# Kernel tuning notes

Hardware: AMD Instinct MI355X
Metric: run time of the kernel (lower is better)

The kernel has to match this reference:

```python
import jax, jax.numpy as jnp
import numpy as np

D_MODEL = 1024
NUM_HEADS = 16
DEPTH = D_MODEL // NUM_HEADS
B, S = 4, 1024


def setup_inputs() -> dict:
    key = jax.random.key(0)
    ks = jax.random.split(key, 9)
    scale = 0.02
    return {
        "v": jax.random.normal(ks[0], (B, S, D_MODEL), jnp.float32),
        "k": jax.random.normal(ks[1], (B, S, D_MODEL), jnp.float32),
        "q": jax.random.normal(ks[2], (B, S, D_MODEL), jnp.float32),
        "wq_w": jax.random.normal(ks[3], (D_MODEL, D_MODEL), jnp.float32) * scale,
        "wq_b": jax.random.normal(ks[4], (D_MODEL,), jnp.float32) * scale,
        "wv_w": jax.random.normal(ks[5], (D_MODEL, D_MODEL), jnp.float32) * scale,
        "wv_b": jax.random.normal(ks[6], (D_MODEL,), jnp.float32) * scale,
        "dense_w": jax.random.normal(ks[7], (D_MODEL, D_MODEL), jnp.float32) * scale,
        "dense_b": jax.random.normal(ks[8], (D_MODEL,), jnp.float32) * scale,
    }


def _split_heads(x):
    # [B, S, D] -> [B, H, S, depth]
    b, s, _ = x.shape
    return x.reshape(b, s, NUM_HEADS, DEPTH).transpose(0, 2, 1, 3)


def reference(v, k, q, wq_w, wq_b, wv_w, wv_b, dense_w, dense_b):
    # Faithful to original torch module, including its bugs:
    #   v = wv(v); k = wv(v)  (k input and wk layer unused)
    #   output = logits @ v   (raw logits, NOT softmax weights)
    del k  # unused in original forward (overwritten)
    q_p = q @ wq_w.T + wq_b
    v_p = v @ wv_w.T + wv_b
    k_p = v_p @ wv_w.T + wv_b  # k = self.wv(v) after v already projected

    qh = _split_heads(q_p)  # [B,H,S,dh]
    kh = _split_heads(k_p)
    vh = _split_heads(v_p)

    logits = jnp.einsum("bhsd,bhtd->bhst", qh, kh) / jnp.sqrt(
        jnp.asarray(DEPTH, jnp.float32)
    )  # [B,H,S,S]
    attention_weights = jax.nn.softmax(logits, axis=-1)
    # BUG preserved: uses logits, not attention_weights
    attn_out = jnp.einsum("bhst,bhtd->bhsd", logits, vh)  # [B,H,S,dh]

    concat = attn_out.transpose(0, 2, 1, 3).reshape(B, S, D_MODEL)
    output = concat @ dense_w.T + dense_b
    # dropout is identity in eval mode
    return output, attention_weights
```

## Files before the change

### kernel.cpp

```cpp
#include <hip/hip_runtime.h>
#include <hip/hip_bf16.h>

#define DM 1024
#define BS 4
#define SS 1024
#define NH 16

typedef __attribute__((ext_vector_type(8))) short bf16x8;
typedef __attribute__((ext_vector_type(4))) float f32x4;

__device__ inline unsigned short f2bf(float x) {
    union { float f; unsigned u; } v; v.f = x;
    unsigned r = v.u + 0x7fffu + ((v.u >> 16) & 1u);
    return (unsigned short)(r >> 16);
}
__device__ inline float bf2f(unsigned short u) {
    union { unsigned u; float f; } v; v.u = ((unsigned)u) << 16;
    return v.f;
}

template<typename T> __device__ inline void store1(T* p, float v);
template<> __device__ inline void store1<float>(float* p, float v) { *p = v; }
template<> __device__ inline void store1<unsigned short>(unsigned short* p, float v) { *p = f2bf(v); }

__device__ inline void glds16(const unsigned short* g, unsigned short* l) {
    __builtin_amdgcn_global_load_lds(
        (const __attribute__((address_space(1))) unsigned int*)g,
        (__attribute__((address_space(3))) unsigned int*)l, 16, 0, 0);
}

__device__ inline void cvt4(const float* src, unsigned short* dst, long long off) {
    float4 v = reinterpret_cast<const float4*>(src)[off];
    ushort4 o;
    o.x = f2bf(v.x); o.y = f2bf(v.y); o.z = f2bf(v.z); o.w = f2bf(v.w);
    reinterpret_cast<ushort4*>(dst)[off] = o;
}

__global__ __launch_bounds__(256) void cvt4_bf16(
    const float* __restrict__ q, const float* __restrict__ v,
    const float* __restrict__ wq, const float* __restrict__ wv,
    unsigned short* __restrict__ qb, unsigned short* __restrict__ vb,
    unsigned short* __restrict__ wqb, unsigned short* __restrict__ wvb)
{
    const long long NQ = (long long)BS * SS * DM / 4;
    const long long NW = (long long)DM * DM / 4;
    const long long total = 2 * NQ + 2 * NW;
    long long i = (long long)blockIdx.x * 256 + threadIdx.x;
    const long long stride = (long long)gridDim.x * 256;
    for (; i < total; i += stride) {
        if (i < NQ)                cvt4(q, qb, i);
        else if (i < 2 * NQ)       cvt4(v, vb, i - NQ);
        else if (i < 2 * NQ + NW)  cvt4(wq, wqb, i - 2 * NQ);
        else                       cvt4(wv, wvb, i - 2 * NQ - NW);
    }
}

__global__ __launch_bounds__(256) void cvt_bf16(const float* __restrict__ in,
                                                unsigned short* __restrict__ out, int n4)
{
    int i = blockIdx.x * blockDim.x + threadIdx.x;
    const int stride = gridDim.x * blockDim.x;
    for (; i < n4; i += stride) cvt4(in, out, i);
}

template<typename TO>
__global__ __launch_bounds__(256) void gemmb_bt(
    const unsigned short* __restrict__ A, int lda, long long sAb, long long sAh,
    const unsigned short* __restrict__ B, int ldb, long long sBb, long long sBh,
    TO* __restrict__ C, int ldc, long long sCb, long long sCh,
    const float* __restrict__ bias, int K, int H, float scale)
{
    __shared__ unsigned short lA[2][128 * 64];
    __shared__ unsigned short lB[2][64 * 64];

    const int tid = threadIdx.x;
    const int wid = tid >> 6, lane = tid & 63;
    const int wr = wid >> 1, wc = wid & 1;
    const int r0 = lane & 15;
    const int kq = (lane >> 4) * 8;
    const int srow = lane >> 3;
    const int scol = (lane & 7) * 8;

    const int z = blockIdx.z, zb = z / H, zh = z % H;
    const unsigned short* Ap = A + sAb * zb + sAh * zh
        + ((long long)blockIdx.y * 128 + srow) * lda + scol;
    const unsigned short* Bp = B + sBb * zb + sBh * zh
        + ((long long)blockIdx.x * 64 + srow) * ldb + scol;
    TO* Cp = C + sCb * zb + sCh * zh
        + (long long)blockIdx.y * 128 * ldc + blockIdx.x * 64;

    f32x4 acc[4][2];
    #pragma unroll
    for (int m = 0; m < 4; ++m)
        #pragma unroll
        for (int n = 0; n < 2; ++n)
            acc[m][n] = f32x4{0.f, 0.f, 0.f, 0.f};

    #pragma unroll
    for (int k = 0; k < 4; ++k)
        glds16(Ap + (long long)(wid * 32 + k * 8) * lda, &lA[0][(wid * 32 + k * 8) * 64]);
    #pragma unroll
    for (int k = 0; k < 2; ++k)
        glds16(Bp + (long long)(wid * 16 + k * 8) * ldb, &lB[0][(wid * 16 + k * 8) * 64]);
    __syncthreads();

    const int NT = K / 64;
    int cur = 0;
    for (int t = 0; t < NT; ++t) {
        if (t + 1 < NT) {
            #pragma unroll
            for (int k = 0; k < 4; ++k)
                glds16(Ap + (long long)(wid * 32 + k * 8) * lda + (t + 1) * 64,
                       &lA[cur ^ 1][(wid * 32 + k * 8) * 64]);
            #pragma unroll
            for (int k = 0; k < 2; ++k)
                glds16(Bp + (long long)(wid * 16 + k * 8) * ldb + (t + 1) * 64,
                       &lB[cur ^ 1][(wid * 16 + k * 8) * 64]);
        }
        #pragma unroll
        for (int ks = 0; ks < 2; ++ks) {
            bf16x8 af[4], bfr[2];
            #pragma unroll
            for (int m = 0; m < 4; ++m)
                af[m] = *reinterpret_cast<const bf16x8*>(
                    &lA[cur][(wr * 64 + m * 16 + r0) * 64 + ks * 32 + kq]);
            #pragma unroll
            for (int n = 0; n < 2; ++n)
                bfr[n] = *reinterpret_cast<const bf16x8*>(
                    &lB[cur][(wc * 32 + n * 16 + r0) * 64 + ks * 32 + kq]);
            #pragma unroll
            for (int m = 0; m < 4; ++m)
                #pragma unroll
                for (int n = 0; n < 2; ++n)
                    acc[m][n] = __builtin_amdgcn_mfma_f32_16x16x32_bf16(af[m], bfr[n], acc[m][n], 0, 0, 0);
        }
        __syncthreads();
        cur ^= 1;
    }

    const int cf = lane & 15, rf = (lane >> 4) * 4;
    #pragma unroll
    for (int m = 0; m < 4; ++m) {
        #pragma unroll
        for (int n = 0; n < 2; ++n) {
            int col = wc * 32 + n * 16 + cf;
            float bv = bias ? bias[blockIdx.x * 64 + col] : 0.0f;
            #pragma unroll
            for (int j = 0; j < 4; ++j) {
                int row = wr * 64 + m * 16 + rf + j;
                store1<TO>(&Cp[(long long)row * ldc + col], acc[m][n][j] * scale + bv);
            }
        }
    }
}

__global__ __launch_bounds__(256) void transpose_vh(const unsigned short* __restrict__ vp,
                                                    unsigned short* __restrict__ vT)
{
    __shared__ unsigned short tile[64][65];
    const int bh = blockIdx.y;
    const int b = bh >> 4, h = bh & 15;
    const long long t0 = (long long)blockIdx.x * 64;
    const int tid = threadIdx.x;
    #pragma unroll
    for (int kk = 0; kk < 4; ++kk) {
        int l = tid + kk * 256;
        int row = l >> 4, c4 = l & 15;
        const unsigned short* src = vp + ((long long)b * SS + t0 + row) * DM + h * 64 + c4 * 4;
        ushort4 val = *reinterpret_cast<const ushort4*>(src);
        tile[row][c4 * 4 + 0] = val.x;
        tile[row][c4 * 4 + 1] = val.y;
        tile[row][c4 * 4 + 2] = val.z;
        tile[row][c4 * 4 + 3] = val.w;
    }
    __syncthreads();
    #pragma unroll
    for (int kk = 0; kk < 4; ++kk) {
        int l = tid + kk * 256;
        int d = l >> 4, i4 = l & 15;
        ushort4 o;
        o.x = tile[i4 * 4 + 0][d];
        o.y = tile[i4 * 4 + 1][d];
        o.z = tile[i4 * 4 + 2][d];
        o.w = tile[i4 * 4 + 3][d];
        *reinterpret_cast<ushort4*>(vT + ((long long)bh * 64 + d) * SS + t0 + i4 * 4) = o;
    }
}

__global__ __launch_bounds__(512, 4) void fused_attn7(
    const unsigned short* __restrict__ qp,
    const unsigned short* __restrict__ kp,
    const unsigned short* __restrict__ vT,
    float* __restrict__ attnw,
    unsigned short* __restrict__ cc)
{
    constexpr int LSTR = 1032;
    __shared__ alignas(16) unsigned short S16[32 * LSTR];
    __shared__ float sW[8][32];
    __shared__ float rowI[32];

    const int tid = threadIdx.x;
    const int w = tid >> 6;
    const int lane = tid & 63;
    const int lg = lane >> 4;
    const int ln = lane & 15;
    const int z = blockIdx.y, b = z >> 4, h = z & 15;
    const int row0 = blockIdx.x * 32;

    const unsigned short* qbase = qp + ((long long)b * SS + row0) * DM + h * 64;
    const unsigned short* kbase = kp + (long long)b * SS * DM + h * 64;
    const unsigned short* vbase = vT + (long long)z * 64 * SS;

    bf16x8 qf[2][2];
    #pragma unroll
    for (int rh = 0; rh < 2; ++rh)
        #pragma unroll
        for (int ks = 0; ks < 2; ++ks)
            qf[rh][ks] = *reinterpret_cast<const bf16x8*>(
                qbase + (long long)(rh * 16 + ln) * DM + ks * 32 + lg * 8);

    float s4[2][4];
    #pragma unroll
    for (int rh = 0; rh < 2; ++rh)
        #pragma unroll
        for (int j = 0; j < 4; ++j) s4[rh][j] = 0.f;

    bf16x8 kf_cur[4];
    #pragma unroll
    for (int i = 0; i < 4; ++i) {
        const int ks = i >> 1, cf2 = i & 1;
        kf_cur[i] = *reinterpret_cast<const bf16x8*>(
            kbase + (long long)(w * 32 + cf2 * 16 + ln) * DM + ks * 32 + lg * 8);
    }
    for (int c = 0; c < 4; ++c) {
        bf16x8 kf_nxt[4];
        if (c < 3) {
            #pragma unroll
            for (int i = 0; i < 4; ++i) {
                const int ks = i >> 1, cf2 = i & 1;
                kf_nxt[i] = *reinterpret_cast<const bf16x8*>(
                    kbase + (long long)((c + 1) * 256 + w * 32 + cf2 * 16 + ln) * DM + ks * 32 + lg * 8);
            }
        }
        f32x4 sac[2][2];
        #pragma unroll
        for (int rh = 0; rh < 2; ++rh) {
            sac[rh][0] = f32x4{0.f, 0.f, 0.f, 0.f};
            sac[rh][1] = f32x4{0.f, 0.f, 0.f, 0.f};
        }
        #pragma unroll
        for (int ks = 0; ks < 2; ++ks)
            #pragma unroll
            for (int cf2 = 0; cf2 < 2; ++cf2)
                #pragma unroll
                for (int rh = 0; rh < 2; ++rh)
                    sac[rh][cf2] = __builtin_amdgcn_mfma_f32_16x16x32_bf16(
                        qf[rh][ks], kf_cur[ks * 2 + cf2], sac[rh][cf2], 0, 0, 0);

        const int colbase = c * 256 + w * 32;
        #pragma unroll
        for (int rh = 0; rh < 2; ++rh) {
            #pragma unroll
            for (int cf2 = 0; cf2 < 2; ++cf2)
                #pragma unroll
                for (int j = 0; j < 4; ++j) {
                    unsigned short ub = f2bf(sac[rh][cf2][j] * 0.125f);
                    S16[(rh * 16 + lg * 4 + j) * LSTR + colbase + cf2 * 16 + ln] = ub;
                    sac[rh][cf2][j] = bf2f(ub);
                }
            #pragma unroll
            for (int j = 0; j < 4; ++j)
                s4[rh][j] += __expf(sac[rh][0][j]) + __expf(sac[rh][1][j]);
        }
        if (c < 3) {
            #pragma unroll
            for (int i = 0; i < 4; ++i) kf_cur[i] = kf_nxt[i];
        }
    }

    #pragma unroll
    for (int rh = 0; rh < 2; ++rh)
        #pragma unroll
        for (int j = 0; j < 4; ++j) {
            #pragma unroll
            for (int o = 1; o < 16; o <<= 1)
                s4[rh][j] += __shfl_xor(s4[rh][j], o);
        }
    if (ln == 0) {
        #pragma unroll
        for (int rh = 0; rh < 2; ++rh)
            #pragma unroll
            for (int j = 0; j < 4; ++j)
                sW[w][rh * 16 + lg * 4 + j] = s4[rh][j];
    }
    __syncthreads();
    if (tid < 32) {
        float sf = 0.f;
        #pragma unroll
        for (int w2 = 0; w2 < 8; ++w2) sf += sW[w2][tid];
        rowI[tid] = 1.0f / sf;
    }
    __syncthreads();

    {
        const int rh = w >> 2, ds = w & 3;
        f32x4 pvn = f32x4{0.f, 0.f, 0.f, 0.f};
        const unsigned short* vrow = vbase + (long long)(ds * 16 + ln) * SS;
        for (int kk = 0; kk < 32; ++kk) {
            bf16x8 sa = *reinterpret_cast<const bf16x8*>(&S16[(rh * 16 + ln) * LSTR + kk * 32 + lg * 8]);
            bf16x8 vf = *reinterpret_cast<const bf16x8*>(vrow + kk * 32 + lg * 8);
            pvn = __builtin_amdgcn_mfma_f32_16x16x32_bf16(sa, vf, pvn, 0, 0, 0);
        }
        #pragma unroll
        for (int j = 0; j < 4; ++j)
            cc[((long long)b * SS + row0 + rh * 16 + lg * 4 + j) * DM + h * 64 + ds * 16 + ln] = f2bf(pvn[j]);
    }

    {
        const int rr = tid >> 8;
        const int tcol = tid & 255;
        #pragma unroll 4
        for (int it = 0; it < 16; ++it) {
            const int row = it * 2 + rr;
            float inv = rowI[row];
            uint2 sv = *reinterpret_cast<const uint2*>(&S16[row * LSTR + tcol * 4]);
            f32x4 o;
            o[0] = __expf(bf2f((unsigned short)(sv.x & 0xffffu))) * inv;
            o[1] = __expf(bf2f((unsigned short)(sv.x >> 16))) * inv;
            o[2] = __expf(bf2f((unsigned short)(sv.y & 0xffffu))) * inv;
            o[3] = __expf(bf2f((unsigned short)(sv.y >> 16))) * inv;
            __builtin_nontemporal_store(
                o, reinterpret_cast<f32x4*>(attnw + ((long long)z * SS + row0 + row) * SS + tcol * 4));
        }
    }
}

extern "C" void kernel_launch(void* const* d_in, const int* in_sizes, int n_in,
                              void* d_out, int out_size, void* d_ws, size_t ws_size,
                              hipStream_t stream) {
    (void)in_sizes; (void)n_in; (void)out_size;
    const float* v    = (const float*)d_in[0];
    const float* q    = (const float*)d_in[2];
    const float* wq_w = (const float*)d_in[3];
    const float* wq_b = (const float*)d_in[4];
    const float* wv_w = (const float*)d_in[5];
    const float* wv_b = (const float*)d_in[6];
    const float* dw   = (const float*)d_in[7];
    const float* db   = (const float*)d_in[8];

    unsigned short* q_p = (unsigned short*)d_ws;
    unsigned short* v_p = q_p + (4 << 20);
    unsigned short* k_p = v_p + (4 << 20);
    unsigned short* vT  = k_p + (4 << 20);
    unsigned short* cc  = vT  + (4 << 20);

    float* out0   = (float*)d_out;
    float* attnw  = out0 + (long long)BS * SS * DM;

    unsigned short* qb  = (unsigned short*)attnw;
    unsigned short* vb  = qb  + (4 << 20);
    unsigned short* wqb = vb  + (4 << 20);
    unsigned short* wvb = wqb + (1 << 20);

    const bool big_ws = ws_size >= (size_t)(42u << 20);
    unsigned short* dwb = big_ws ? (cc + (4 << 20)) : q_p;

    dim3 blk(256);
    dim3 projGrid(DM / 64, BS * SS / 128, 1);

    cvt4_bf16<<<dim3(2048), blk, 0, stream>>>(q, v, wq_w, wv_w, qb, vb, wqb, wvb);
    if (big_ws)
        cvt_bf16<<<dim3(256), blk, 0, stream>>>(dw, dwb, (DM * DM) / 4);

    gemmb_bt<unsigned short><<<projGrid, blk, 0, stream>>>(
        qb, DM, 0, 0, wqb, DM, 0, 0, q_p, DM, 0, 0, wq_b, DM, 1, 1.0f);
    gemmb_bt<unsigned short><<<projGrid, blk, 0, stream>>>(
        vb, DM, 0, 0, wvb, DM, 0, 0, v_p, DM, 0, 0, wv_b, DM, 1, 1.0f);
    gemmb_bt<unsigned short><<<projGrid, blk, 0, stream>>>(
        v_p, DM, 0, 0, wvb, DM, 0, 0, k_p, DM, 0, 0, wv_b, DM, 1, 1.0f);

    transpose_vh<<<dim3(16, 64), blk, 0, stream>>>(v_p, vT);

    fused_attn7<<<dim3(SS / 32, BS * NH), dim3(512), 0, stream>>>(q_p, k_p, vT, attnw, cc);

    if (!big_ws)
        cvt_bf16<<<dim3(256), blk, 0, stream>>>(dw, dwb, (DM * DM) / 4);
    gemmb_bt<float><<<projGrid, blk, 0, stream>>>(
        cc, DM, 0, 0, dwb, DM, 0, 0, out0, DM, 0, 0, db, DM, 1, 1.0f);
}
```

Measured before the change: 221.9 us.

## Batch Q and V projections into one 128x128-tile GEMM launch

Adds a 512-thread GEMM kernel with 128x128 output tiles and a z-dimension batch index, so the Q and V projections run together in one launch. This relies on the contiguous workspace layout of inputs, weights and outputs, and on copying both biases into a combined buffer. The aim is to cut launch count, raise reuse per tile and fill the GPU with a larger grid. The cost is higher LDS and register use per block, a larger workspace requirement (threshold raised to 43 MB), and a fallback path of two separate launches when the workspace is small. The transpose is also moved ahead of the K projection.

```diff
diff --git a/kernel.cpp b/kernel.cpp
--- a/kernel.cpp
+++ b/kernel.cpp
@@ -61,6 +61,93 @@
     int i = blockIdx.x * blockDim.x + threadIdx.x;
     const int stride = gridDim.x * blockDim.x;
     for (; i < n4; i += stride) cvt4(in, out, i);
+}
+
+template<typename TO>
+__global__ __launch_bounds__(512) void gemm128_bt(
+    const unsigned short* __restrict__ A, int lda, long long sAh,
+    const unsigned short* __restrict__ B, int ldb, long long sBh,
+    TO* __restrict__ C, int ldc, long long sCh,
+    const float* __restrict__ bias, long long sBiasH, int K, float scale)
+{
+    __shared__ unsigned short lA[2][128 * 64];
+    __shared__ unsigned short lB[2][128 * 64];
+
+    const int tid = threadIdx.x;
+    const int wid = tid >> 6, lane = tid & 63;
+    const int wr = wid >> 2, wc = wid & 3;
+    const int r0 = lane & 15;
+    const int kq = (lane >> 4) * 8;
+    const int srow = lane >> 3;
+    const int scol = (lane & 7) * 8;
+
+    const int z = blockIdx.z;
+    const unsigned short* Ap = A + sAh * z + ((long long)blockIdx.y * 128 + srow) * lda + scol;
+    const unsigned short* Bp = B + sBh * z + ((long long)blockIdx.x * 128 + srow) * ldb + scol;
+    TO* Cp = C + sCh * z + (long long)blockIdx.y * 128 * ldc + blockIdx.x * 128;
+    const float* bp = bias + sBiasH * z + blockIdx.x * 128;
+
+    f32x4 acc[4][2];
+    #pragma unroll
+    for (int m = 0; m < 4; ++m)
+        #pragma unroll
+        for (int n = 0; n < 2; ++n)
+            acc[m][n] = f32x4{0.f, 0.f, 0.f, 0.f};
+
+    #pragma unroll
+    for (int k = 0; k < 2; ++k) {
+        glds16(Ap + (long long)(wid * 16 + k * 8) * lda, &lA[0][(wid * 16 + k * 8) * 64]);
+        glds16(Bp + (long long)(wid * 16 + k * 8) * ldb, &lB[0][(wid * 16 + k * 8) * 64]);
+    }
+    __syncthreads();
+
+    const int NT = K / 64;
+    int cur = 0;
+    for (int t = 0; t < NT; ++t) {
+        if (t + 1 < NT) {
+            #pragma unroll
+            for (int k = 0; k < 2; ++k) {
+                glds16(Ap + (long long)(wid * 16 + k * 8) * lda + (t + 1) * 64,
+                       &lA[cur ^ 1][(wid * 16 + k * 8) * 64]);
+                glds16(Bp + (long long)(wid * 16 + k * 8) * ldb + (t + 1) * 64,
+                       &lB[cur ^ 1][(wid * 16 + k * 8) * 64]);
+            }
+        }
+        #pragma unroll
+        for (int ks = 0; ks < 2; ++ks) {
+            bf16x8 af[4], bfr[2];
+            #pragma unroll
+            for (int m = 0; m < 4; ++m)
+                af[m] = *reinterpret_cast<const bf16x8*>(
+                    &lA[cur][(wr * 64 + m * 16 + r0) * 64 + ks * 32 + kq]);
+            #pragma unroll
+            for (int n = 0; n < 2; ++n)
+                bfr[n] = *reinterpret_cast<const bf16x8*>(
+                    &lB[cur][(wc * 32 + n * 16 + r0) * 64 + ks * 32 + kq]);
+            #pragma unroll
+            for (int m = 0; m < 4; ++m)
+                #pragma unroll
+                for (int n = 0; n < 2; ++n)
+                    acc[m][n] = __builtin_amdgcn_mfma_f32_16x16x32_bf16(af[m], bfr[n], acc[m][n], 0, 0, 0);
+        }
+        __syncthreads();
+        cur ^= 1;
+    }
+
+    const int cf = lane & 15, rf = (lane >> 4) * 4;
+    #pragma unroll
+    for (int m = 0; m < 4; ++m) {
+        #pragma unroll
+        for (int n = 0; n < 2; ++n) {
+            int col = wc * 32 + n * 16 + cf;
+            float bv = bp[col];
+            #pragma unroll
+            for (int j = 0; j < 4; ++j) {
+                int row = wr * 64 + m * 16 + rf + j;
+                store1<TO>(&Cp[(long long)row * ldc + col], acc[m][n][j] * scale + bv);
+            }
+        }
+    }
 }
 
 template<typename TO>
@@ -362,29 +449,39 @@
     unsigned short* wqb = vb  + (4 << 20);
     unsigned short* wvb = wqb + (1 << 20);
 
-    const bool big_ws = ws_size >= (size_t)(42u << 20);
+    const bool big_ws = ws_size >= (size_t)(43u << 20);
     unsigned short* dwb = big_ws ? (cc + (4 << 20)) : q_p;
+    float* biasQV = big_ws ? (float*)(dwb + (1 << 20)) : nullptr;
 
     dim3 blk(256);
-    dim3 projGrid(DM / 64, BS * SS / 128, 1);
 
     cvt4_bf16<<<dim3(2048), blk, 0, stream>>>(q, v, wq_w, wv_w, qb, vb, wqb, wvb);
-    if (big_ws)
+    if (big_ws) {
         cvt_bf16<<<dim3(256), blk, 0, stream>>>(dw, dwb, (DM * DM) / 4);
-
-    gemmb_bt<unsigned short><<<projGrid, blk, 0, stream>>>(
-        qb, DM, 0, 0, wqb, DM, 0, 0, q_p, DM, 0, 0, wq_b, DM, 1, 1.0f);
-    gemmb_bt<unsigned short><<<projGrid, blk, 0, stream>>>(
-        vb, DM, 0, 0, wvb, DM, 0, 0, v_p, DM, 0, 0, wv_b, DM, 1, 1.0f);
-    gemmb_bt<unsigned short><<<projGrid, blk, 0, stream>>>(
+        hipMemcpyAsync(biasQV, wq_b, DM * sizeof(float), hipMemcpyDeviceToDevice, stream);
+        hipMemcpyAsync(biasQV + DM, wv_b, DM * sizeof(float), hipMemcpyDeviceToDevice, stream);
+    }
+
+    if (big_ws) {
+        gemm128_bt<unsigned short><<<dim3(DM / 128, BS * SS / 128, 2), dim3(512), 0, stream>>>(
+            qb, DM, (long long)(4 << 20), wqb, DM, (long long)(1 << 20),
+            q_p, DM, (long long)(4 << 20), biasQV, DM, DM, 1.0f);
+    } else {
+        gemm128_bt<unsigned short><<<dim3(DM / 128, BS * SS / 128, 1), dim3(512), 0, stream>>>(
+            qb, DM, 0, wqb, DM, 0, q_p, DM, 0, wq_b, 0, DM, 1.0f);
+        gemm128_bt<unsigned short><<<dim3(DM / 128, BS * SS / 128, 1), dim3(512), 0, stream>>>(
+            vb, DM, 0, wvb, DM, 0, v_p, DM, 0, wv_b, 0, DM, 1.0f);
+    }
+
+    transpose_vh<<<dim3(16, 64), blk, 0, stream>>>(v_p, vT);
+
+    gemmb_bt<unsigned short><<<dim3(DM / 64, BS * SS / 128, 1), blk, 0, stream>>>(
         v_p, DM, 0, 0, wvb, DM, 0, 0, k_p, DM, 0, 0, wv_b, DM, 1, 1.0f);
-
-    transpose_vh<<<dim3(16, 64), blk, 0, stream>>>(v_p, vT);
 
     fused_attn7<<<dim3(SS / 32, BS * NH), dim3(512), 0, stream>>>(q_p, k_p, vT, attnw, cc);
 
     if (!big_ws)
         cvt_bf16<<<dim3(256), blk, 0, stream>>>(dw, dwb, (DM * DM) / 4);
-    gemmb_bt<float><<<projGrid, blk, 0, stream>>>(
+    gemmb_bt<float><<<dim3(DM / 64, BS * SS / 128, 1), blk, 0, stream>>>(
         cc, DM, 0, 0, dwb, DM, 0, 0, out0, DM, 0, 0, db, DM, 1, 1.0f);
 }
```

New measurement: 212.7 us, median of 2. 4.1% less time.

## Use 128x128 GEMM tiles, batch Q/V projections, stage K in LDS for attention

Applied to the files above, without the earlier changes.

Replaces the 128x64 projection GEMM with a 512-thread 128x128-tile kernel and runs the Q and V projections in a single launch via a z-batched grid with a concatenated bias buffer. The attention kernel is reworked to 16-row blocks of 256 threads that double-buffer K chunks into swizzled LDS through direct global-to-LDS loads instead of per-lane register loads. The aim is more reuse per tile, fewer launches and better-coalesced K access. In exchange, each attention block handles fewer rows, so K is reread more often overall, and the workspace threshold grows.

```diff
diff --git a/kernel.cpp b/kernel.cpp
--- a/kernel.cpp
+++ b/kernel.cpp
@@ -64,30 +64,28 @@
 }
 
 template<typename TO>
-__global__ __launch_bounds__(256) void gemmb_bt(
-    const unsigned short* __restrict__ A, int lda, long long sAb, long long sAh,
-    const unsigned short* __restrict__ B, int ldb, long long sBb, long long sBh,
-    TO* __restrict__ C, int ldc, long long sCb, long long sCh,
-    const float* __restrict__ bias, int K, int H, float scale)
+__global__ __launch_bounds__(512) void gemm128_bt(
+    const unsigned short* __restrict__ A, int lda, long long sAh,
+    const unsigned short* __restrict__ B, int ldb, long long sBh,
+    TO* __restrict__ C, int ldc, long long sCh,
+    const float* __restrict__ bias, long long sBiasH, int K, float scale)
 {
     __shared__ unsigned short lA[2][128 * 64];
-    __shared__ unsigned short lB[2][64 * 64];
+    __shared__ unsigned short lB[2][128 * 64];
 
     const int tid = threadIdx.x;
     const int wid = tid >> 6, lane = tid & 63;
-    const int wr = wid >> 1, wc = wid & 1;
+    const int wr = wid >> 2, wc = wid & 3;
     const int r0 = lane & 15;
     const int kq = (lane >> 4) * 8;
     const int srow = lane >> 3;
     const int scol = (lane & 7) * 8;
 
-    const int z = blockIdx.z, zb = z / H, zh = z % H;
-    const unsigned short* Ap = A + sAb * zb + sAh * zh
-        + ((long long)blockIdx.y * 128 + srow) * lda + scol;
-    const unsigned short* Bp = B + sBb * zb + sBh * zh
-        + ((long long)blockIdx.x * 64 + srow) * ldb + scol;
-    TO* Cp = C + sCb * zb + sCh * zh
-        + (long long)blockIdx.y * 128 * ldc + blockIdx.x * 64;
+    const int z = blockIdx.z;
+    const unsigned short* Ap = A + sAh * z + ((long long)blockIdx.y * 128 + srow) * lda + scol;
+    const unsigned short* Bp = B + sBh * z + ((long long)blockIdx.x * 128 + srow) * ldb + scol;
+    TO* Cp = C + sCh * z + (long long)blockIdx.y * 128 * ldc + blockIdx.x * 128;
+    const float* bp = bias + sBiasH * z + blockIdx.x * 128;
 
     f32x4 acc[4][2];
     #pragma unroll
@@ -97,11 +95,10 @@
             acc[m][n] = f32x4{0.f, 0.f, 0.f, 0.f};
 
     #pragma unroll
-    for (int k = 0; k < 4; ++k)
-        glds16(Ap + (long long)(wid * 32 + k * 8) * lda, &lA[0][(wid * 32 + k * 8) * 64]);
-    #pragma unroll
-    for (int k = 0; k < 2; ++k)
+    for (int k = 0; k < 2; ++k) {
+        glds16(Ap + (long long)(wid * 16 + k * 8) * lda, &lA[0][(wid * 16 + k * 8) * 64]);
         glds16(Bp + (long long)(wid * 16 + k * 8) * ldb, &lB[0][(wid * 16 + k * 8) * 64]);
+    }
     __syncthreads();
 
     const int NT = K / 64;
@@ -109,13 +106,12 @@
     for (int t = 0; t < NT; ++t) {
         if (t + 1 < NT) {
             #pragma unroll
-            for (int k = 0; k < 4; ++k)
-                glds16(Ap + (long long)(wid * 32 + k * 8) * lda + (t + 1) * 64,
-                       &lA[cur ^ 1][(wid * 32 + k * 8) * 64]);
-            #pragma unroll
-            for (int k = 0; k < 2; ++k)
+            for (int k = 0; k < 2; ++k) {
+                glds16(Ap + (long long)(wid * 16 + k * 8) * lda + (t + 1) * 64,
+                       &lA[cur ^ 1][(wid * 16 + k * 8) * 64]);
                 glds16(Bp + (long long)(wid * 16 + k * 8) * ldb + (t + 1) * 64,
                        &lB[cur ^ 1][(wid * 16 + k * 8) * 64]);
+            }
         }
         #pragma unroll
         for (int ks = 0; ks < 2; ++ks) {
@@ -144,7 +140,7 @@
         #pragma unroll
         for (int n = 0; n < 2; ++n) {
             int col = wc * 32 + n * 16 + cf;
-            float bv = bias ? bias[blockIdx.x * 64 + col] : 0.0f;
+            float bv = bp[col];
             #pragma unroll
             for (int j = 0; j < 4; ++j) {
                 int row = wr * 64 + m * 16 + rf + j;
@@ -187,7 +183,7 @@
     }
 }
 
-__global__ __launch_bounds__(512, 4) void fused_attn7(
+__global__ __launch_bounds__(256) void fused_attn8(
     const unsigned short* __restrict__ qp,
     const unsigned short* __restrict__ kp,
     const unsigned short* __restrict__ vT,
@@ -195,9 +191,10 @@
     unsigned short* __restrict__ cc)
 {
     constexpr int LSTR = 1032;
-    __shared__ alignas(16) unsigned short S16[32 * LSTR];
-    __shared__ float sW[8][32];
-    __shared__ float rowI[32];
+    __shared__ alignas(16) unsigned short S16[16 * LSTR];
+    __shared__ alignas(16) unsigned short Kst[2][128 * 64];
+    __shared__ float sW[4][16];
+    __shared__ float rowI[16];
 
     const int tid = threadIdx.x;
     const int w = tid >> 6;
@@ -205,134 +202,112 @@
     const int lg = lane >> 4;
     const int ln = lane & 15;
     const int z = blockIdx.y, b = z >> 4, h = z & 15;
-    const int row0 = blockIdx.x * 32;
+    const int row0 = blockIdx.x * 16;
 
     const unsigned short* qbase = qp + ((long long)b * SS + row0) * DM + h * 64;
     const unsigned short* kbase = kp + (long long)b * SS * DM + h * 64;
     const unsigned short* vbase = vT + (long long)z * 64 * SS;
 
-    bf16x8 qf[2][2];
-    #pragma unroll
-    for (int rh = 0; rh < 2; ++rh)
-        #pragma unroll
-        for (int ks = 0; ks < 2; ++ks)
-            qf[rh][ks] = *reinterpret_cast<const bf16x8*>(
-                qbase + (long long)(rh * 16 + ln) * DM + ks * 32 + lg * 8);
-
-    float s4[2][4];
-    #pragma unroll
-    for (int rh = 0; rh < 2; ++rh)
-        #pragma unroll
-        for (int j = 0; j < 4; ++j) s4[rh][j] = 0.f;
-
-    bf16x8 kf_cur[4];
-    #pragma unroll
-    for (int i = 0; i < 4; ++i) {
-        const int ks = i >> 1, cf2 = i & 1;
-        kf_cur[i] = *reinterpret_cast<const bf16x8*>(
-            kbase + (long long)(w * 32 + cf2 * 16 + ln) * DM + ks * 32 + lg * 8);
-    }
-    for (int c = 0; c < 4; ++c) {
-        bf16x8 kf_nxt[4];
-        if (c < 3) {
-            #pragma unroll
-            for (int i = 0; i < 4; ++i) {
-                const int ks = i >> 1, cf2 = i & 1;
-                kf_nxt[i] = *reinterpret_cast<const bf16x8*>(
-                    kbase + (long long)((c + 1) * 256 + w * 32 + cf2 * 16 + ln) * DM + ks * 32 + lg * 8);
+    bf16x8 qf[2];
+    #pragma unroll
+    for (int ks = 0; ks < 2; ++ks)
+        qf[ks] = *reinterpret_cast<const bf16x8*>(qbase + (long long)ln * DM + ks * 32 + lg * 8);
+
+    const int lrow = lane >> 3;
+    const int gslot = (lane & 7) ^ lrow;
+
+#define STAGE_K(c_, buf_)                                                            \
+    {                                                                                \
+        const unsigned short* kc_ = kbase                                            \
+            + (long long)((c_) * 128 + w * 32 + lrow) * DM + gslot * 8;              \
+        _Pragma("unroll")                                                            \
+        for (int k_ = 0; k_ < 4; ++k_)                                               \
+            glds16(kc_ + (long long)(k_ * 8) * DM, &Kst[buf_][(w * 32 + k_ * 8) * 64]); \
+    }
+
+    STAGE_K(0, 0);
+    __syncthreads();
+
+    float s4[4];
+    #pragma unroll
+    for (int j = 0; j < 4; ++j) s4[j] = 0.f;
+
+    int cur = 0;
+    for (int c = 0; c < 8; ++c) {
+        if (c < 7) STAGE_K(c + 1, cur ^ 1);
+
+        f32x4 sac[2];
+        sac[0] = f32x4{0.f, 0.f, 0.f, 0.f};
+        sac[1] = f32x4{0.f, 0.f, 0.f, 0.f};
+        #pragma unroll
+        for (int ks = 0; ks < 2; ++ks) {
+            #pragma unroll
+            for (int cf2 = 0; cf2 < 2; ++cf2) {
+                const int rloc = w * 32 + cf2 * 16 + ln;
+                bf16x8 kf = *reinterpret_cast<const bf16x8*>(
+                    &Kst[cur][(rloc * 8 + ((ks * 4 + lg) ^ (ln & 7))) * 8]);
+                sac[cf2] = __builtin_amdgcn_mfma_f32_16x16x32_bf16(qf[ks], kf, sac[cf2], 0, 0, 0);
             }
         }
-        f32x4 sac[2][2];
-        #pragma unroll
-        for (int rh = 0; rh < 2; ++rh) {
-            sac[rh][0] = f32x4{0.f, 0.f, 0.f, 0.f};
-            sac[rh][1] = f32x4{0.f, 0.f, 0.f, 0.f};
-        }
-        #pragma unroll
-        for (int ks = 0; ks < 2; ++ks)
-            #pragma unroll
-            for (int cf2 = 0; cf2 < 2; ++cf2)
-                #pragma unroll
-                for (int rh = 0; rh < 2; ++rh)
-                    sac[rh][cf2] = __builtin_amdgcn_mfma_f32_16x16x32_bf16(
-                        qf[rh][ks], kf_cur[ks * 2 + cf2], sac[rh][cf2], 0, 0, 0);
-
-        const int colbase = c * 256 + w * 32;
-        #pragma unroll
-        for (int rh = 0; rh < 2; ++rh) {
-            #pragma unroll
-            for (int cf2 = 0; cf2 < 2; ++cf2)
-                #pragma unroll
-                for (int j = 0; j < 4; ++j) {
-                    unsigned short ub = f2bf(sac[rh][cf2][j] * 0.125f);
-                    S16[(rh * 16 + lg * 4 + j) * LSTR + colbase + cf2 * 16 + ln] = ub;
-                    sac[rh][cf2][j] = bf2f(ub);
-                }
-            #pragma unroll
-            for (int j = 0; j < 4; ++j)
-                s4[rh][j] += __expf(sac[rh][0][j]) + __expf(sac[rh][1][j]);
-        }
-        if (c < 3) {
-            #pragma unroll
-            for (int i = 0; i < 4; ++i) kf_cur[i] = kf_nxt[i];
-        }
-    }
-
-    #pragma unroll
-    for (int rh = 0; rh < 2; ++rh)
-        #pragma unroll
-        for (int j = 0; j < 4; ++j) {
-            #pragma unroll
-            for (int o = 1; o < 16; o <<= 1)
-                s4[rh][j] += __shfl_xor(s4[rh][j], o);
-        }
+
+        const int colbase = c * 128 + w * 32;
+        #pragma unroll
+        for (int cf2 = 0; cf2 < 2; ++cf2)
+            #pragma unroll
+            for (int j = 0; j < 4; ++j) {
+                unsigned short ub = f2bf(sac[cf2][j] * 0.125f);
+                S16[(lg * 4 + j) * LSTR + colbase + cf2 * 16 + ln] = ub;
+                sac[cf2][j] = bf2f(ub);
+            }
+        #pragma unroll
+        for (int j = 0; j < 4; ++j)
+            s4[j] += __expf(sac[0][j]) + __expf(sac[1][j]);
+
+        __syncthreads();
+        cur ^= 1;
+    }
+
+    #pragma unroll
+    for (int j = 0; j < 4; ++j) {
+        #pragma unroll
+        for (int o = 1; o < 16; o <<= 1)
+            s4[j] += __shfl_xor(s4[j], o);
+    }
     if (ln == 0) {
         #pragma unroll
-        for (int rh = 0; rh < 2; ++rh)
-            #pragma unroll
-            for (int j = 0; j < 4; ++j)
-                sW[w][rh * 16 + lg * 4 + j] = s4[rh][j];
-    }
-    __syncthreads();
-    if (tid < 32) {
-        float sf = 0.f;
-        #pragma unroll
-        for (int w2 = 0; w2 < 8; ++w2) sf += sW[w2][tid];
-        rowI[tid] = 1.0f / sf;
-    }
+        for (int j = 0; j < 4; ++j) sW[w][lg * 4 + j] = s4[j];
+    }
+    __syncthreads();
+    if (tid < 16)
+        rowI[tid] = 1.0f / (sW[0][tid] + sW[1][tid] + sW[2][tid] + sW[3][tid]);
     __syncthreads();
 
     {
-        const int rh = w >> 2, ds = w & 3;
         f32x4 pvn = f32x4{0.f, 0.f, 0.f, 0.f};
-        const unsigned short* vrow = vbase + (long long)(ds * 16 + ln) * SS;
+        const unsigned short* vrow = vbase + (long long)(w * 16 + ln) * SS;
         for (int kk = 0; kk < 32; ++kk) {
-            bf16x8 sa = *reinterpret_cast<const bf16x8*>(&S16[(rh * 16 + ln) * LSTR + kk * 32 + lg * 8]);
+            bf16x8 sa = *reinterpret_cast<const bf16x8*>(&S16[ln * LSTR + kk * 32 + lg * 8]);
             bf16x8 vf = *reinterpret_cast<const bf16x8*>(vrow + kk * 32 + lg * 8);
             pvn = __builtin_amdgcn_mfma_f32_16x16x32_bf16(sa, vf, pvn, 0, 0, 0);
         }
         #pragma unroll
         for (int j = 0; j < 4; ++j)
-            cc[((long long)b * SS + row0 + rh * 16 + lg * 4 + j) * DM + h * 64 + ds * 16 + ln] = f2bf(pvn[j]);
-    }
-
-    {
-        const int rr = tid >> 8;
-        const int tcol = tid & 255;
-        #pragma unroll 4
-        for (int it = 0; it < 16; ++it) {
-            const int row = it * 2 + rr;
-            float inv = rowI[row];
-            uint2 sv = *reinterpret_cast<const uint2*>(&S16[row * LSTR + tcol * 4]);
-            f32x4 o;
-            o[0] = __expf(bf2f((unsigned short)(sv.x & 0xffffu))) * inv;
-            o[1] = __expf(bf2f((unsigned short)(sv.x >> 16))) * inv;
-            o[2] = __expf(bf2f((unsigned short)(sv.y & 0xffffu))) * inv;
-            o[3] = __expf(bf2f((unsigned short)(sv.y >> 16))) * inv;
-            __builtin_nontemporal_store(
-                o, reinterpret_cast<f32x4*>(attnw + ((long long)z * SS + row0 + row) * SS + tcol * 4));
-        }
-    }
+            cc[((long long)b * SS + row0 + lg * 4 + j) * DM + h * 64 + w * 16 + ln] = f2bf(pvn[j]);
+    }
+
+    #pragma unroll 4
+    for (int it = 0; it < 16; ++it) {
+        float inv = rowI[it];
+        uint2 sv = *reinterpret_cast<const uint2*>(&S16[it * LSTR + tid * 4]);
+        f32x4 o;
+        o[0] = __expf(bf2f((unsigned short)(sv.x & 0xffffu))) * inv;
+        o[1] = __expf(bf2f((unsigned short)(sv.x >> 16))) * inv;
+        o[2] = __expf(bf2f((unsigned short)(sv.y & 0xffffu))) * inv;
+        o[3] = __expf(bf2f((unsigned short)(sv.y >> 16))) * inv;
+        __builtin_nontemporal_store(
+            o, reinterpret_cast<f32x4*>(attnw + ((long long)z * SS + row0 + it) * SS + tid * 4));
+    }
+#undef STAGE_K
 }
 
 extern "C" void kernel_launch(void* const* d_in, const int* in_sizes, int n_in,
@@ -362,29 +337,39 @@
     unsigned short* wqb = vb  + (4 << 20);
     unsigned short* wvb = wqb + (1 << 20);
 
-    const bool big_ws = ws_size >= (size_t)(42u << 20);
+    const bool big_ws = ws_size >= (size_t)(43u << 20);
     unsigned short* dwb = big_ws ? (cc + (4 << 20)) : q_p;
+    float* biasQV = big_ws ? (float*)(dwb + (1 << 20)) : nullptr;
 
     dim3 blk(256);
-    dim3 projGrid(DM / 64, BS * SS / 128, 1);
 
     cvt4_bf16<<<dim3(2048), blk, 0, stream>>>(q, v, wq_w, wv_w, qb, vb, wqb, wvb);
-    if (big_ws)
+    if (big_ws) {
         cvt_bf16<<<dim3(256), blk, 0, stream>>>(dw, dwb, (DM * DM) / 4);
-
-    gemmb_bt<unsigned short><<<projGrid, blk, 0, stream>>>(
-        qb, DM, 0, 0, wqb, DM, 0, 0, q_p, DM, 0, 0, wq_b, DM, 1, 1.0f);
-    gemmb_bt<unsigned short><<<projGrid, blk, 0, stream>>>(
-        vb, DM, 0, 0, wvb, DM, 0, 0, v_p, DM, 0, 0, wv_b, DM, 1, 1.0f);
-    gemmb_bt<unsigned short><<<projGrid, blk, 0, stream>>>(
-        v_p, DM, 0, 0, wvb, DM, 0, 0, k_p, DM, 0, 0, wv_b, DM, 1, 1.0f);
+        hipMemcpyAsync(biasQV, wq_b, DM * sizeof(float), hipMemcpyDeviceToDevice, stream);
+        hipMemcpyAsync(biasQV + DM, wv_b, DM * sizeof(float), hipMemcpyDeviceToDevice, stream);
+    }
+
+    if (big_ws) {
+        gemm128_bt<unsigned short><<<dim3(DM / 128, BS * SS / 128, 2), dim3(512), 0, stream>>>(
+            qb, DM, (long long)(4 << 20), wqb, DM, (long long)(1 << 20),
+            q_p, DM, (long long)(4 << 20), biasQV, DM, DM, 1.0f);
+    } else {
+        gemm128_bt<unsigned short><<<dim3(DM / 128, BS * SS / 128, 1), dim3(512), 0, stream>>>(
+            qb, DM, 0, wqb, DM, 0, q_p, DM, 0, wq_b, 0, DM, 1.0f);
+        gemm128_bt<unsigned short><<<dim3(DM / 128, BS * SS / 128, 1), dim3(512), 0, stream>>>(
+            vb, DM, 0, wvb, DM, 0, v_p, DM, 0, wv_b, 0, DM, 1.0f);
+    }
 
     transpose_vh<<<dim3(16, 64), blk, 0, stream>>>(v_p, vT);
 
-    fused_attn7<<<dim3(SS / 32, BS * NH), dim3(512), 0, stream>>>(q_p, k_p, vT, attnw, cc);
+    gemm128_bt<unsigned short><<<dim3(DM / 128, BS * SS / 128, 1), dim3(512), 0, stream>>>(
+        v_p, DM, 0, wvb, DM, 0, k_p, DM, 0, wv_b, 0, DM, 1.0f);
+
+    fused_attn8<<<dim3(SS / 16, BS * NH), blk, 0, stream>>>(q_p, k_p, vT, attnw, cc);
 
     if (!big_ws)
         cvt_bf16<<<dim3(256), blk, 0, stream>>>(dw, dwb, (DM * DM) / 4);
-    gemmb_bt<float><<<projGrid, blk, 0, stream>>>(
-        cc, DM, 0, 0, dwb, DM, 0, 0, out0, DM, 0, 0, db, DM, 1, 1.0f);
-}
+    gemm128_bt<float><<<dim3(DM / 128, BS * SS / 128, 1), dim3(512), 0, stream>>>(
+        cc, DM, 0, dwb, DM, 0, out0, DM, 0, db, 0, DM, 1.0f);
+}
```

Measured after the change: 236.9 us. +6.8%, slower.

## Use 128x128 GEMM tiles, batch Q/V projections, fuse dense weight conversion

Applied to the files above, without the earlier changes.

The projection GEMM becomes a 512-thread kernel with 128x128 output tiles, which improves operand reuse per loaded tile. When workspace allows, the Q and V projections run as one batched launch, with the biases copied into a contiguous buffer so each batch slice has its own bias. The dense-weight conversion is folded into the main conversion kernel, and the attention grid is remapped so consecutive blocks spread across heads. These changes cut launch count and improve tile reuse, at the cost of a larger workspace requirement and fewer, larger blocks per GEMM.

```diff
diff --git a/kernel.cpp b/kernel.cpp
--- a/kernel.cpp
+++ b/kernel.cpp
@@ -36,22 +36,25 @@
     reinterpret_cast<ushort4*>(dst)[off] = o;
 }
 
-__global__ __launch_bounds__(256) void cvt4_bf16(
+__global__ __launch_bounds__(256) void cvt5_bf16(
     const float* __restrict__ q, const float* __restrict__ v,
     const float* __restrict__ wq, const float* __restrict__ wv,
+    const float* __restrict__ dw,
     unsigned short* __restrict__ qb, unsigned short* __restrict__ vb,
-    unsigned short* __restrict__ wqb, unsigned short* __restrict__ wvb)
+    unsigned short* __restrict__ wqb, unsigned short* __restrict__ wvb,
+    unsigned short* __restrict__ dwb)
 {
     const long long NQ = (long long)BS * SS * DM / 4;
     const long long NW = (long long)DM * DM / 4;
-    const long long total = 2 * NQ + 2 * NW;
+    const long long total = 2 * NQ + 2 * NW + (dw ? NW : 0);
     long long i = (long long)blockIdx.x * 256 + threadIdx.x;
     const long long stride = (long long)gridDim.x * 256;
     for (; i < total; i += stride) {
-        if (i < NQ)                cvt4(q, qb, i);
-        else if (i < 2 * NQ)       cvt4(v, vb, i - NQ);
-        else if (i < 2 * NQ + NW)  cvt4(wq, wqb, i - 2 * NQ);
-        else                       cvt4(wv, wvb, i - 2 * NQ - NW);
+        if (i < NQ)                     cvt4(q, qb, i);
+        else if (i < 2 * NQ)            cvt4(v, vb, i - NQ);
+        else if (i < 2 * NQ + NW)       cvt4(wq, wqb, i - 2 * NQ);
+        else if (i < 2 * NQ + 2 * NW)   cvt4(wv, wvb, i - 2 * NQ - NW);
+        else                            cvt4(dw, dwb, i - 2 * NQ - 2 * NW);
     }
 }
 
@@ -64,30 +67,28 @@
 }
 
 template<typename TO>
-__global__ __launch_bounds__(256) void gemmb_bt(
-    const unsigned short* __restrict__ A, int lda, long long sAb, long long sAh,
-    const unsigned short* __restrict__ B, int ldb, long long sBb, long long sBh,
-    TO* __restrict__ C, int ldc, long long sCb, long long sCh,
-    const float* __restrict__ bias, int K, int H, float scale)
+__global__ __launch_bounds__(512) void gemm128_bt(
+    const unsigned short* __restrict__ A, int lda, long long sAh,
+    const unsigned short* __restrict__ B, int ldb, long long sBh,
+    TO* __restrict__ C, int ldc, long long sCh,
+    const float* __restrict__ bias, long long sBiasH, int K, float scale)
 {
     __shared__ unsigned short lA[2][128 * 64];
-    __shared__ unsigned short lB[2][64 * 64];
+    __shared__ unsigned short lB[2][128 * 64];
 
     const int tid = threadIdx.x;
     const int wid = tid >> 6, lane = tid & 63;
-    const int wr = wid >> 1, wc = wid & 1;
+    const int wr = wid >> 2, wc = wid & 3;
     const int r0 = lane & 15;
     const int kq = (lane >> 4) * 8;
     const int srow = lane >> 3;
     const int scol = (lane & 7) * 8;
 
-    const int z = blockIdx.z, zb = z / H, zh = z % H;
-    const unsigned short* Ap = A + sAb * zb + sAh * zh
-        + ((long long)blockIdx.y * 128 + srow) * lda + scol;
-    const unsigned short* Bp = B + sBb * zb + sBh * zh
-        + ((long long)blockIdx.x * 64 + srow) * ldb + scol;
-    TO* Cp = C + sCb * zb + sCh * zh
-        + (long long)blockIdx.y * 128 * ldc + blockIdx.x * 64;
+    const int z = blockIdx.z;
+    const unsigned short* Ap = A + sAh * z + ((long long)blockIdx.y * 128 + srow) * lda + scol;
+    const unsigned short* Bp = B + sBh * z + ((long long)blockIdx.x * 128 + srow) * ldb + scol;
+    TO* Cp = C + sCh * z + (long long)blockIdx.y * 128 * ldc + blockIdx.x * 128;
+    const float* bp = bias + sBiasH * z + blockIdx.x * 128;
 
     f32x4 acc[4][2];
     #pragma unroll
@@ -97,11 +98,10 @@
             acc[m][n] = f32x4{0.f, 0.f, 0.f, 0.f};
 
     #pragma unroll
-    for (int k = 0; k < 4; ++k)
-        glds16(Ap + (long long)(wid * 32 + k * 8) * lda, &lA[0][(wid * 32 + k * 8) * 64]);
-    #pragma unroll
-    for (int k = 0; k < 2; ++k)
+    for (int k = 0; k < 2; ++k) {
+        glds16(Ap + (long long)(wid * 16 + k * 8) * lda, &lA[0][(wid * 16 + k * 8) * 64]);
         glds16(Bp + (long long)(wid * 16 + k * 8) * ldb, &lB[0][(wid * 16 + k * 8) * 64]);
+    }
     __syncthreads();
 
     const int NT = K / 64;
@@ -109,13 +109,12 @@
     for (int t = 0; t < NT; ++t) {
         if (t + 1 < NT) {
             #pragma unroll
-            for (int k = 0; k < 4; ++k)
-                glds16(Ap + (long long)(wid * 32 + k * 8) * lda + (t + 1) * 64,
-                       &lA[cur ^ 1][(wid * 32 + k * 8) * 64]);
-            #pragma unroll
-            for (int k = 0; k < 2; ++k)
+            for (int k = 0; k < 2; ++k) {
+                glds16(Ap + (long long)(wid * 16 + k * 8) * lda + (t + 1) * 64,
+                       &lA[cur ^ 1][(wid * 16 + k * 8) * 64]);
                 glds16(Bp + (long long)(wid * 16 + k * 8) * ldb + (t + 1) * 64,
                        &lB[cur ^ 1][(wid * 16 + k * 8) * 64]);
+            }
         }
         #pragma unroll
         for (int ks = 0; ks < 2; ++ks) {
@@ -144,7 +143,7 @@
         #pragma unroll
         for (int n = 0; n < 2; ++n) {
             int col = wc * 32 + n * 16 + cf;
-            float bv = bias ? bias[blockIdx.x * 64 + col] : 0.0f;
+            float bv = bp[col];
             #pragma unroll
             for (int j = 0; j < 4; ++j) {
                 int row = wr * 64 + m * 16 + rf + j;
@@ -204,8 +203,12 @@
     const int lane = tid & 63;
     const int lg = lane >> 4;
     const int ln = lane & 15;
-    const int z = blockIdx.y, b = z >> 4, h = z & 15;
-    const int row0 = blockIdx.x * 32;
+
+    const int raw = blockIdx.x + (SS / 32) * blockIdx.y;
+    const int id2 = (raw & 7) * 256 + (raw >> 3);
+    const int z = id2 >> 5;
+    const int row0 = (id2 & 31) * 32;
+    const int b = z >> 4, h = z & 15;
 
     const unsigned short* qbase = qp + ((long long)b * SS + row0) * DM + h * 64;
     const unsigned short* kbase = kp + (long long)b * SS * DM + h * 64;
@@ -362,29 +365,39 @@
     unsigned short* wqb = vb  + (4 << 20);
     unsigned short* wvb = wqb + (1 << 20);
 
-    const bool big_ws = ws_size >= (size_t)(42u << 20);
+    const bool big_ws = ws_size >= (size_t)(43u << 20);
     unsigned short* dwb = big_ws ? (cc + (4 << 20)) : q_p;
+    float* biasQV = big_ws ? (float*)(dwb + (1 << 20)) : nullptr;
 
     dim3 blk(256);
-    dim3 projGrid(DM / 64, BS * SS / 128, 1);
-
-    cvt4_bf16<<<dim3(2048), blk, 0, stream>>>(q, v, wq_w, wv_w, qb, vb, wqb, wvb);
-    if (big_ws)
-        cvt_bf16<<<dim3(256), blk, 0, stream>>>(dw, dwb, (DM * DM) / 4);
-
-    gemmb_bt<unsigned short><<<projGrid, blk, 0, stream>>>(
-        qb, DM, 0, 0, wqb, DM, 0, 0, q_p, DM, 0, 0, wq_b, DM, 1, 1.0f);
-    gemmb_bt<unsigned short><<<projGrid, blk, 0, stream>>>(
-        vb, DM, 0, 0, wvb, DM, 0, 0, v_p, DM, 0, 0, wv_b, DM, 1, 1.0f);
-    gemmb_bt<unsigned short><<<projGrid, blk, 0, stream>>>(
-        v_p, DM, 0, 0, wvb, DM, 0, 0, k_p, DM, 0, 0, wv_b, DM, 1, 1.0f);
+
+    cvt5_bf16<<<dim3(2048), blk, 0, stream>>>(
+        q, v, wq_w, wv_w, big_ws ? dw : nullptr, qb, vb, wqb, wvb, dwb);
+    if (big_ws) {
+        hipMemcpyAsync(biasQV, wq_b, DM * sizeof(float), hipMemcpyDeviceToDevice, stream);
+        hipMemcpyAsync(biasQV + DM, wv_b, DM * sizeof(float), hipMemcpyDeviceToDevice, stream);
+    }
+
+    if (big_ws) {
+        gemm128_bt<unsigned short><<<dim3(DM / 128, BS * SS / 128, 2), dim3(512), 0, stream>>>(
+            qb, DM, (long long)(4 << 20), wqb, DM, (long long)(1 << 20),
+            q_p, DM, (long long)(4 << 20), biasQV, DM, DM, 1.0f);
+    } else {
+        gemm128_bt<unsigned short><<<dim3(DM / 128, BS * SS / 128, 1), dim3(512), 0, stream>>>(
+            qb, DM, 0, wqb, DM, 0, q_p, DM, 0, wq_b, 0, DM, 1.0f);
+        gemm128_bt<unsigned short><<<dim3(DM / 128, BS * SS / 128, 1), dim3(512), 0, stream>>>(
+            vb, DM, 0, wvb, DM, 0, v_p, DM, 0, wv_b, 0, DM, 1.0f);
+    }
 
     transpose_vh<<<dim3(16, 64), blk, 0, stream>>>(v_p, vT);
+
+    gemm128_bt<unsigned short><<<dim3(DM / 128, BS * SS / 128, 1), dim3(512), 0, stream>>>(
+        v_p, DM, 0, wvb, DM, 0, k_p, DM, 0, wv_b, 0, DM, 1.0f);
 
     fused_attn7<<<dim3(SS / 32, BS * NH), dim3(512), 0, stream>>>(q_p, k_p, vT, attnw, cc);
 
     if (!big_ws)
         cvt_bf16<<<dim3(256), blk, 0, stream>>>(dw, dwb, (DM * DM) / 4);
-    gemmb_bt<float><<<projGrid, blk, 0, stream>>>(
-        cc, DM, 0, 0, dwb, DM, 0, 0, out0, DM, 0, 0, db, DM, 1, 1.0f);
-}
+    gemm128_bt<float><<<dim3(DM / 128, BS * SS / 128, 1), dim3(512), 0, stream>>>(
+        cc, DM, 0, dwb, DM, 0, out0, DM, 0, db, 0, DM, 1.0f);
+}
```

After: 216.7 us. -2.3%, faster.
